# Kernel optimization log

Measured on AMD Instinct MI355X. Metric: run time of the kernel, lower is better.

The kernel has to match this reference:

```python
import jax, jax.numpy as jnp
import numpy as np

N_NODES = 100000
N_EDGES = 6400000


def _gcn_conv(x, src, dst, W, b, num_nodes):
    # GCNConv: x' = D^{-1/2} (A + I) D^{-1/2} X W + b
    # (src/dst already include self-loops; deg computed on A+I at dst, PyG default flow)
    h = x @ W  # [N, out]
    ones = jnp.ones(src.shape[0], dtype=h.dtype)
    deg = jax.ops.segment_sum(ones, dst, num_segments=num_nodes)  # in-degree incl. self-loops
    dinv = jnp.where(deg > 0, deg ** -0.5, 0.0)  # [N]
    norm = dinv[src] * dinv[dst]  # [E]
    msg = h[src] * norm[:, None]  # gather + scale, [E, out]
    agg = jax.ops.segment_sum(msg, dst, num_segments=num_nodes)  # scatter-add, [N, out]
    return agg + b


def setup_inputs() -> dict:
    key = jax.random.key(0)
    k1, k2, k3, k4 = jax.random.split(key, 4)
    x = jax.random.normal(k1, (N_NODES, 1), dtype=jnp.float32)
    edge_index = jax.random.randint(k2, (2, N_EDGES), 0, N_NODES, dtype=jnp.int64)
    # Glorot-style init for GCN weights
    W1 = jax.random.normal(k3, (1, 16), dtype=jnp.float32) * (2.0 / (1 + 16)) ** 0.5
    b1 = jnp.zeros((16,), dtype=jnp.float32)
    W2 = jax.random.normal(k4, (16, 2), dtype=jnp.float32) * (2.0 / (16 + 2)) ** 0.5
    b2 = jnp.zeros((2,), dtype=jnp.float32)
    return {"x": x, "edge_index": edge_index, "W1": W1, "b1": b1, "W2": W2, "b2": b2}


def reference(x, edge_index, W1, b1, W2, b2):
    num_nodes = x.shape[0]
    loops = jnp.arange(num_nodes, dtype=edge_index.dtype)
    src = jnp.concatenate([edge_index[0], loops])
    dst = jnp.concatenate([edge_index[1], loops])
    h = jax.nn.relu(_gcn_conv(x, src, dst, W1, b1, num_nodes))
    # F.dropout with training=False (eval) is identity
    out = _gcn_conv(h, src, dst, W2, b2, num_nodes)
    return jax.nn.log_softmax(out, axis=1)
```

## Files before the change

### kernel.cpp

```cpp
#include <hip/hip_runtime.h>
#include <hip/hip_fp16.h>

#define TPB 256
#define LOG_NPB 9
#define NPB 512
#define SPLIT 16
#define CHUNK 4096
#define RCAP 44


__device__ __forceinline__ void lds_pk_add_f16(unsigned* addr, unsigned val) {
  asm volatile("ds_pk_add_f16 %0, %1"
               :: "v"((unsigned)(unsigned long long)addr), "v"(val)
               : "memory");
}

__global__ void k_reset(int* __restrict__ gcur, int K) {
  int i = blockIdx.x * blockDim.x + threadIdx.x;
  if (i < K) gcur[i] = 0;
}

__global__ __launch_bounds__(TPB) void
k_bucket(const int* __restrict__ src, const int* __restrict__ dst,
         int E, int K, int capG,
         int* __restrict__ gcur, unsigned int* __restrict__ packed) {
  extern __shared__ unsigned smem[];
  unsigned* stage = smem;
  int* cur = (int*)(smem + (size_t)K * RCAP);
  int* res = cur + K;

  const int t = threadIdx.x;
  const int e0 = blockIdx.x * CHUNK;
  const int e1 = min(e0 + CHUNK, E);

  for (int b = t; b < K; b += TPB) cur[b] = 0;
  __syncthreads();

  for (int base = e0 + 4 * t; base < e1; base += 4 * TPB) {
    if (base + 4 <= e1) {
      int4 dv = *reinterpret_cast<const int4*>(dst + base);
      int4 sv = *reinterpret_cast<const int4*>(src + base);
      int d[4] = {dv.x, dv.y, dv.z, dv.w};
      int s[4] = {sv.x, sv.y, sv.z, sv.w};
#pragma unroll
      for (int j = 0; j < 4; ++j) {
        int b = d[j] >> LOG_NPB;
        unsigned pk = ((unsigned)s[j] << LOG_NPB) | (unsigned)(d[j] & (NPB - 1));
        int p = atomicAdd(&cur[b], 1);
        if (p < RCAP) {
          stage[b * RCAP + p] = pk;
        } else {
          int gp = atomicAdd(&gcur[b], 1);
          if (gp < capG) packed[(size_t)b * capG + gp] = pk;
        }
      }
    } else {
      for (int j = 0; j < 4; ++j) {
        int idx = base + j;
        if (idx < e1) {
          int d = dst[idx], s = src[idx];
          int b = d >> LOG_NPB;
          unsigned pk = ((unsigned)s << LOG_NPB) | (unsigned)(d & (NPB - 1));
          int p = atomicAdd(&cur[b], 1);
          if (p < RCAP) {
            stage[b * RCAP + p] = pk;
          } else {
            int gp = atomicAdd(&gcur[b], 1);
            if (gp < capG) packed[(size_t)b * capG + gp] = pk;
          }
        }
      }
    }
  }
  __syncthreads();

  if (t < K) {
    int c = min(cur[t], RCAP);
    res[t] = (c > 0) ? atomicAdd(&gcur[t], c) : 0;
  }
  __syncthreads();

  const int tot = K * RCAP;
  for (int i = t; i < tot; i += TPB) {
    int b = i / RCAP;
    int pos = i - b * RCAP;
    if (pos < min(cur[b], RCAP)) {
      int gp = res[b] + pos;
      if (gp < capG) packed[(size_t)b * capG + gp] = stage[i];
    }
  }
}

__device__ __forceinline__ void slice_range(int cnt, int s, int& off0, int& off1) {
  off0 = (int)(((long long)cnt * s) / SPLIT) & ~3;
  off1 = (s == SPLIT - 1) ? cnt : (int)(((long long)cnt * (s + 1)) / SPLIT) & ~3;
}

__global__ __launch_bounds__(TPB) void
k_deg(const unsigned int* __restrict__ packed, const int* __restrict__ gcur,
      int cap, int* __restrict__ pdeg, int Npad) {
  int b = blockIdx.x / SPLIT, s = blockIdx.x % SPLIT;
  __shared__ int bins[NPB];
  for (int i = threadIdx.x; i < NPB; i += TPB) bins[i] = 0;
  __syncthreads();
  int cnt = min(gcur[b], cap);
  int off0, off1; slice_range(cnt, s, off0, off1);
  const unsigned int* base = packed + (size_t)b * cap;
  int len = off1 - off0;
  int nfull = len >> 3;
  for (int g = threadIdx.x; g < nfull; g += TPB) {
    int e = off0 + (g << 3);
    uint4 pa = *reinterpret_cast<const uint4*>(base + e);
    uint4 pb = *reinterpret_cast<const uint4*>(base + e + 4);
    atomicAdd(&bins[pa.x & (NPB - 1)], 1);
    atomicAdd(&bins[pa.y & (NPB - 1)], 1);
    atomicAdd(&bins[pa.z & (NPB - 1)], 1);
    atomicAdd(&bins[pa.w & (NPB - 1)], 1);
    atomicAdd(&bins[pb.x & (NPB - 1)], 1);
    atomicAdd(&bins[pb.y & (NPB - 1)], 1);
    atomicAdd(&bins[pb.z & (NPB - 1)], 1);
    atomicAdd(&bins[pb.w & (NPB - 1)], 1);
  }
  for (int e = off0 + (nfull << 3) + threadIdx.x; e < off1; e += TPB)
    atomicAdd(&bins[base[e] & (NPB - 1)], 1);
  __syncthreads();
  int nb = b << LOG_NPB;
  for (int i = threadIdx.x; i < NPB; i += TPB)
    pdeg[s * Npad + nb + i] = bins[i];
}

__global__ void k_dinv(const int* __restrict__ pdeg, const float* __restrict__ x,
                       float* __restrict__ dinv, float* __restrict__ xd,
                       int N, int Npad) {
  int i = blockIdx.x * TPB + threadIdx.x;
  if (i >= N) return;
  int d = 1;
#pragma unroll
  for (int s = 0; s < SPLIT; ++s) d += pdeg[s * Npad + i];
  float di = rsqrtf((float)d);
  dinv[i] = di;
  xd[i] = x[i] * di;
}

__global__ __launch_bounds__(TPB) void
k_pass1(const unsigned int* __restrict__ packed, const int* __restrict__ gcur,
        int cap, const float* __restrict__ xd, float* __restrict__ pt1, int Npad) {
  int b = blockIdx.x / SPLIT, s = blockIdx.x % SPLIT;
  __shared__ float bins[NPB];
  for (int i = threadIdx.x; i < NPB; i += TPB) bins[i] = 0.f;
  __syncthreads();
  int cnt = min(gcur[b], cap);
  int off0, off1; slice_range(cnt, s, off0, off1);
  const unsigned int* base = packed + (size_t)b * cap;
  int len = off1 - off0;
  int nfull = len >> 3;
  for (int g = threadIdx.x; g < nfull; g += TPB) {
    int e = off0 + (g << 3);
    uint4 pa = *reinterpret_cast<const uint4*>(base + e);
    uint4 pb = *reinterpret_cast<const uint4*>(base + e + 4);
    float v0 = xd[pa.x >> LOG_NPB];
    float v1 = xd[pa.y >> LOG_NPB];
    float v2 = xd[pa.z >> LOG_NPB];
    float v3 = xd[pa.w >> LOG_NPB];
    float v4 = xd[pb.x >> LOG_NPB];
    float v5 = xd[pb.y >> LOG_NPB];
    float v6 = xd[pb.z >> LOG_NPB];
    float v7 = xd[pb.w >> LOG_NPB];
    atomicAdd(&bins[pa.x & (NPB - 1)], v0);
    atomicAdd(&bins[pa.y & (NPB - 1)], v1);
    atomicAdd(&bins[pa.z & (NPB - 1)], v2);
    atomicAdd(&bins[pa.w & (NPB - 1)], v3);
    atomicAdd(&bins[pb.x & (NPB - 1)], v4);
    atomicAdd(&bins[pb.y & (NPB - 1)], v5);
    atomicAdd(&bins[pb.z & (NPB - 1)], v6);
    atomicAdd(&bins[pb.w & (NPB - 1)], v7);
  }
  for (int e = off0 + (nfull << 3) + threadIdx.x; e < off1; e += TPB) {
    unsigned int p = base[e];
    atomicAdd(&bins[p & (NPB - 1)], xd[p >> LOG_NPB]);
  }
  __syncthreads();
  int nb = b << LOG_NPB;
  for (int i = threadIdx.x; i < NPB; i += TPB)
    pt1[s * Npad + nb + i] = bins[i];
}

__global__ void k_node(const float* __restrict__ pt1, const float* __restrict__ xd,
                       const float* __restrict__ dinv,
                       const float* __restrict__ W1, const float* __restrict__ b1,
                       const float* __restrict__ W2,
                       unsigned* __restrict__ gdp, int N, int Npad) {
  int i = blockIdx.x * TPB + threadIdx.x;
  if (i >= N) return;
  float tv = 0.f;
#pragma unroll
  for (int s = 0; s < SPLIT; ++s) tv += pt1[s * Npad + i];
  float di = dinv[i];
  float sv = di * (tv + xd[i]);
  float g0 = 0.f, g1 = 0.f;
#pragma unroll
  for (int j = 0; j < 16; ++j) {
    float h = fmaxf(fmaf(sv, W1[j], b1[j]), 0.f);
    g0 = fmaf(h, W2[2 * j], g0);
    g1 = fmaf(h, W2[2 * j + 1], g1);
  }
  __half2 h2 = __floats2half2_rn(g0 * di, g1 * di);
  gdp[i] = *reinterpret_cast<unsigned*>(&h2);
}

__global__ __launch_bounds__(TPB) void
k_pass2(const unsigned int* __restrict__ packed, const int* __restrict__ gcur,
        int cap, const unsigned* __restrict__ gdp, float* __restrict__ pt2, int Npad) {
  int b = blockIdx.x / SPLIT, s = blockIdx.x % SPLIT;
  __shared__ unsigned bins[NPB];
  for (int i = threadIdx.x; i < NPB; i += TPB) bins[i] = 0u;
  __syncthreads();
  int cnt = min(gcur[b], cap);
  int off0, off1; slice_range(cnt, s, off0, off1);
  const unsigned int* base = packed + (size_t)b * cap;
  int len = off1 - off0;
  int nfull = len >> 3;
  for (int g = threadIdx.x; g < nfull; g += TPB) {
    int e = off0 + (g << 3);
    uint4 pa = *reinterpret_cast<const uint4*>(base + e);
    uint4 pb = *reinterpret_cast<const uint4*>(base + e + 4);
    unsigned v0 = gdp[pa.x >> LOG_NPB];
    unsigned v1 = gdp[pa.y >> LOG_NPB];
    unsigned v2 = gdp[pa.z >> LOG_NPB];
    unsigned v3 = gdp[pa.w >> LOG_NPB];
    unsigned v4 = gdp[pb.x >> LOG_NPB];
    unsigned v5 = gdp[pb.y >> LOG_NPB];
    unsigned v6 = gdp[pb.z >> LOG_NPB];
    unsigned v7 = gdp[pb.w >> LOG_NPB];
    lds_pk_add_f16(&bins[pa.x & (NPB - 1)], v0);
    lds_pk_add_f16(&bins[pa.y & (NPB - 1)], v1);
    lds_pk_add_f16(&bins[pa.z & (NPB - 1)], v2);
    lds_pk_add_f16(&bins[pa.w & (NPB - 1)], v3);
    lds_pk_add_f16(&bins[pb.x & (NPB - 1)], v4);
    lds_pk_add_f16(&bins[pb.y & (NPB - 1)], v5);
    lds_pk_add_f16(&bins[pb.z & (NPB - 1)], v6);
    lds_pk_add_f16(&bins[pb.w & (NPB - 1)], v7);
  }
  for (int e = off0 + (nfull << 3) + threadIdx.x; e < off1; e += TPB) {
    unsigned int p = base[e];
    lds_pk_add_f16(&bins[p & (NPB - 1)], gdp[p >> LOG_NPB]);
  }
  __syncthreads();
  int nb = b << LOG_NPB;
  for (int i = threadIdx.x; i < NPB; i += TPB) {
    __half2 h = *reinterpret_cast<__half2*>(&bins[i]);
    float2 o;
    o.x = __low2float(h);
    o.y = __high2float(h);
    *reinterpret_cast<float2*>(pt2 + (size_t)s * 2 * Npad + 2 * (nb + i)) = o;
  }
}

__global__ void k_final(const float* __restrict__ pt2, const unsigned* __restrict__ gdp,
                        const float* __restrict__ dinv, const float* __restrict__ b2,
                        float* __restrict__ out, int N, int Npad) {
  int i = blockIdx.x * TPB + threadIdx.x;
  if (i >= N) return;
  float t0 = 0.f, t1 = 0.f;
#pragma unroll
  for (int s = 0; s < SPLIT; ++s) {
    float2 p = *reinterpret_cast<const float2*>(pt2 + (size_t)s * 2 * Npad + 2 * i);
    t0 += p.x;
    t1 += p.y;
  }
  unsigned gp = gdp[i];
  __half2 h = *reinterpret_cast<__half2*>(&gp);
  float di = dinv[i];
  float o0 = di * (t0 + __low2float(h)) + b2[0];
  float o1 = di * (t1 + __high2float(h)) + b2[1];
  float m = fmaxf(o0, o1);
  float l = m + logf(expf(o0 - m) + expf(o1 - m));
  out[2 * i] = o0 - l;
  out[2 * i + 1] = o1 - l;
}

extern "C" void kernel_launch(void* const* d_in, const int* in_sizes, int n_in,
                              void* d_out, int out_size, void* d_ws, size_t ws_size,
                              hipStream_t stream) {
  const float* x  = (const float*)d_in[0];
  const int*   ei = (const int*)d_in[1];
  const float* W1 = (const float*)d_in[2];
  const float* b1 = (const float*)d_in[3];
  const float* W2 = (const float*)d_in[4];
  const float* b2 = (const float*)d_in[5];

  const int N = in_sizes[0];
  const int E = in_sizes[1] / 2;
  const int* src = ei;
  const int* dst = ei + E;

  const int K = (N + NPB - 1) >> LOG_NPB;
  const int Npad = K << LOG_NPB;
  int mean = (int)(((long long)E * NPB) / N);
  int cap = mean + mean / 16 + 512;
  cap = (cap + 3) & ~3;

  char* ws = (char*)d_ws;
  auto align256 = [&](size_t n) { char* p = ws; ws += (n + 255) & ~(size_t)255; return p; };

  int*          gcur   = (int*)align256((size_t)K * 4);
  unsigned int* packed = (unsigned int*)align256((size_t)K * cap * 4);
  float*        dinv   = (float*)align256((size_t)N * 4);
  float*        xd     = (float*)align256((size_t)N * 4);
  unsigned*     gdp    = (unsigned*)align256((size_t)N * 4);
  float*        R      = (float*)align256((size_t)SPLIT * 2 * Npad * 4);
  int*          pdeg   = (int*)R;
  float*        pt1    = R;
  float*        pt2    = R;

  float* out = (float*)d_out;

  int nb_node   = (N + TPB - 1) / TPB;
  int nb_bucket = (E + CHUNK - 1) / CHUNK;
  int nb_acc    = K * SPLIT;
  size_t sh_bucket = ((size_t)K * RCAP + 2 * (size_t)K) * 4;

  k_reset <<<(K + TPB - 1) / TPB, TPB, 0, stream>>>(gcur, K);
  k_bucket<<<nb_bucket, TPB, sh_bucket, stream>>>(src, dst, E, K, cap, gcur, packed);
  k_deg   <<<nb_acc, TPB, 0, stream>>>(packed, gcur, cap, pdeg, Npad);
  k_dinv  <<<nb_node, TPB, 0, stream>>>(pdeg, x, dinv, xd, N, Npad);
  k_pass1 <<<nb_acc, TPB, 0, stream>>>(packed, gcur, cap, xd, pt1, Npad);
  k_node  <<<nb_node, TPB, 0, stream>>>(pt1, xd, dinv, W1, b1, W2, gdp, N, Npad);
  k_pass2 <<<nb_acc, TPB, 0, stream>>>(packed, gcur, cap, gdp, pt2, Npad);
  k_final <<<nb_node, TPB, 0, stream>>>(pt2, gdp, dinv, b2, out, N, Npad);
}
```

Baseline: 147.6 us.

## Pack degree and layer-1 partial sums into fp16 pairs with packed LDS atomics

The degree count and the first-layer scatter now accumulate into half2-packed LDS bins using ds_pk_add_f16, so two nodes share each bin word. Per-slice partials are written as packed fp16, which halves partial-buffer traffic in k_deg, k_dinv, k_pass1, k_node and k_final, and the node kernels each handle two nodes. The bucket kernel also loads 8 edges per thread and RCAP drops to 40. The risk is fp16 precision loss: per-slice degree counts are still exact, but the layer-1 partial sums of normalized features are rounded before the cross-slice sum.

New measurement: 174.3 us. 1.18x slower.

```diff
diff --git a/kernel.cpp b/kernel.cpp
--- a/kernel.cpp
+++ b/kernel.cpp
@@ -4,9 +4,10 @@
 #define TPB 256
 #define LOG_NPB 9
 #define NPB 512
+#define HPB 256
 #define SPLIT 16
 #define CHUNK 4096
-#define RCAP 44
+#define RCAP 40
 
 
 __device__ __forceinline__ void lds_pk_add_f16(unsigned* addr, unsigned val) {
@@ -36,14 +37,16 @@
   for (int b = t; b < K; b += TPB) cur[b] = 0;
   __syncthreads();
 
-  for (int base = e0 + 4 * t; base < e1; base += 4 * TPB) {
-    if (base + 4 <= e1) {
-      int4 dv = *reinterpret_cast<const int4*>(dst + base);
-      int4 sv = *reinterpret_cast<const int4*>(src + base);
-      int d[4] = {dv.x, dv.y, dv.z, dv.w};
-      int s[4] = {sv.x, sv.y, sv.z, sv.w};
-#pragma unroll
-      for (int j = 0; j < 4; ++j) {
+  for (int base = e0 + 8 * t; base < e1; base += 8 * TPB) {
+    if (base + 8 <= e1) {
+      int4 dv0 = *reinterpret_cast<const int4*>(dst + base);
+      int4 dv1 = *reinterpret_cast<const int4*>(dst + base + 4);
+      int4 sv0 = *reinterpret_cast<const int4*>(src + base);
+      int4 sv1 = *reinterpret_cast<const int4*>(src + base + 4);
+      int d[8] = {dv0.x, dv0.y, dv0.z, dv0.w, dv1.x, dv1.y, dv1.z, dv1.w};
+      int s[8] = {sv0.x, sv0.y, sv0.z, sv0.w, sv1.x, sv1.y, sv1.z, sv1.w};
+#pragma unroll
+      for (int j = 0; j < 8; ++j) {
         int b = d[j] >> LOG_NPB;
         unsigned pk = ((unsigned)s[j] << LOG_NPB) | (unsigned)(d[j] & (NPB - 1));
         int p = atomicAdd(&cur[b], 1);
@@ -55,19 +58,16 @@
         }
       }
     } else {
-      for (int j = 0; j < 4; ++j) {
-        int idx = base + j;
-        if (idx < e1) {
-          int d = dst[idx], s = src[idx];
-          int b = d >> LOG_NPB;
-          unsigned pk = ((unsigned)s << LOG_NPB) | (unsigned)(d & (NPB - 1));
-          int p = atomicAdd(&cur[b], 1);
-          if (p < RCAP) {
-            stage[b * RCAP + p] = pk;
-          } else {
-            int gp = atomicAdd(&gcur[b], 1);
-            if (gp < capG) packed[(size_t)b * capG + gp] = pk;
-          }
+      for (int idx = base; idx < e1; ++idx) {
+        int d = dst[idx], s = src[idx];
+        int b = d >> LOG_NPB;
+        unsigned pk = ((unsigned)s << LOG_NPB) | (unsigned)(d & (NPB - 1));
+        int p = atomicAdd(&cur[b], 1);
+        if (p < RCAP) {
+          stage[b * RCAP + p] = pk;
+        } else {
+          int gp = atomicAdd(&gcur[b], 1);
+          if (gp < capG) packed[(size_t)b * capG + gp] = pk;
         }
       }
     }
@@ -98,56 +98,65 @@
 
 __global__ __launch_bounds__(TPB) void
 k_deg(const unsigned int* __restrict__ packed, const int* __restrict__ gcur,
-      int cap, int* __restrict__ pdeg, int Npad) {
+      int cap, unsigned* __restrict__ pdeg_pk, int halfNpad) {
   int b = blockIdx.x / SPLIT, s = blockIdx.x % SPLIT;
-  __shared__ int bins[NPB];
-  for (int i = threadIdx.x; i < NPB; i += TPB) bins[i] = 0;
+  __shared__ unsigned binsp[HPB];
+  for (int i = threadIdx.x; i < HPB; i += TPB) binsp[i] = 0u;
   __syncthreads();
   int cnt = min(gcur[b], cap);
   int off0, off1; slice_range(cnt, s, off0, off1);
   const unsigned int* base = packed + (size_t)b * cap;
   int len = off1 - off0;
   int nfull = len >> 3;
+#define DEG1(P) { unsigned l_ = (P) & (NPB - 1); \
+  lds_pk_add_f16(&binsp[l_ >> 1], (l_ & 1) ? 0x3C000000u : 0x00003C00u); }
   for (int g = threadIdx.x; g < nfull; g += TPB) {
     int e = off0 + (g << 3);
     uint4 pa = *reinterpret_cast<const uint4*>(base + e);
     uint4 pb = *reinterpret_cast<const uint4*>(base + e + 4);
-    atomicAdd(&bins[pa.x & (NPB - 1)], 1);
-    atomicAdd(&bins[pa.y & (NPB - 1)], 1);
-    atomicAdd(&bins[pa.z & (NPB - 1)], 1);
-    atomicAdd(&bins[pa.w & (NPB - 1)], 1);
-    atomicAdd(&bins[pb.x & (NPB - 1)], 1);
-    atomicAdd(&bins[pb.y & (NPB - 1)], 1);
-    atomicAdd(&bins[pb.z & (NPB - 1)], 1);
-    atomicAdd(&bins[pb.w & (NPB - 1)], 1);
+    DEG1(pa.x) DEG1(pa.y) DEG1(pa.z) DEG1(pa.w)
+    DEG1(pb.x) DEG1(pb.y) DEG1(pb.z) DEG1(pb.w)
   }
   for (int e = off0 + (nfull << 3) + threadIdx.x; e < off1; e += TPB)
-    atomicAdd(&bins[base[e] & (NPB - 1)], 1);
-  __syncthreads();
-  int nb = b << LOG_NPB;
-  for (int i = threadIdx.x; i < NPB; i += TPB)
-    pdeg[s * Npad + nb + i] = bins[i];
-}
-
-__global__ void k_dinv(const int* __restrict__ pdeg, const float* __restrict__ x,
+    DEG1(base[e])
+#undef DEG1
+  __syncthreads();
+  int nb = b << (LOG_NPB - 1);
+  for (int i = threadIdx.x; i < HPB; i += TPB)
+    pdeg_pk[s * halfNpad + nb + i] = binsp[i];
+}
+
+__global__ void k_dinv(const unsigned* __restrict__ pdeg_pk, const float* __restrict__ x,
                        float* __restrict__ dinv, float* __restrict__ xd,
-                       int N, int Npad) {
-  int i = blockIdx.x * TPB + threadIdx.x;
-  if (i >= N) return;
-  int d = 1;
-#pragma unroll
-  for (int s = 0; s < SPLIT; ++s) d += pdeg[s * Npad + i];
-  float di = rsqrtf((float)d);
-  dinv[i] = di;
-  xd[i] = x[i] * di;
+                       int N, int halfNpad) {
+  int i2 = blockIdx.x * TPB + threadIdx.x;
+  int n0 = 2 * i2;
+  if (n0 >= N) return;
+  float d0 = 1.f, d1 = 1.f;
+#pragma unroll
+  for (int s = 0; s < SPLIT; ++s) {
+    unsigned v = pdeg_pk[s * halfNpad + i2];
+    __half2 h = *reinterpret_cast<__half2*>(&v);
+    d0 += __low2float(h);
+    d1 += __high2float(h);
+  }
+  float di0 = rsqrtf(d0);
+  dinv[n0] = di0;
+  xd[n0] = x[n0] * di0;
+  if (n0 + 1 < N) {
+    float di1 = rsqrtf(d1);
+    dinv[n0 + 1] = di1;
+    xd[n0 + 1] = x[n0 + 1] * di1;
+  }
 }
 
 __global__ __launch_bounds__(TPB) void
 k_pass1(const unsigned int* __restrict__ packed, const int* __restrict__ gcur,
-        int cap, const float* __restrict__ xd, float* __restrict__ pt1, int Npad) {
+        int cap, const float* __restrict__ xd, unsigned* __restrict__ pt1_pk,
+        int halfNpad) {
   int b = blockIdx.x / SPLIT, s = blockIdx.x % SPLIT;
-  __shared__ float bins[NPB];
-  for (int i = threadIdx.x; i < NPB; i += TPB) bins[i] = 0.f;
+  __shared__ unsigned binsp[HPB];
+  for (int i = threadIdx.x; i < HPB; i += TPB) binsp[i] = 0u;
   __syncthreads();
   int cnt = min(gcur[b], cap);
   int off0, off1; slice_range(cnt, s, off0, off1);
@@ -166,51 +175,71 @@
     float v5 = xd[pb.y >> LOG_NPB];
     float v6 = xd[pb.z >> LOG_NPB];
     float v7 = xd[pb.w >> LOG_NPB];
-    atomicAdd(&bins[pa.x & (NPB - 1)], v0);
-    atomicAdd(&bins[pa.y & (NPB - 1)], v1);
-    atomicAdd(&bins[pa.z & (NPB - 1)], v2);
-    atomicAdd(&bins[pa.w & (NPB - 1)], v3);
-    atomicAdd(&bins[pb.x & (NPB - 1)], v4);
-    atomicAdd(&bins[pb.y & (NPB - 1)], v5);
-    atomicAdd(&bins[pb.z & (NPB - 1)], v6);
-    atomicAdd(&bins[pb.w & (NPB - 1)], v7);
+#define P1(P, V) { unsigned l_ = (P) & (NPB - 1); \
+  unsigned hv_ = (unsigned)__half_as_ushort(__float2half(V)); \
+  lds_pk_add_f16(&binsp[l_ >> 1], hv_ << ((l_ & 1) * 16)); }
+    P1(pa.x, v0) P1(pa.y, v1) P1(pa.z, v2) P1(pa.w, v3)
+    P1(pb.x, v4) P1(pb.y, v5) P1(pb.z, v6) P1(pb.w, v7)
   }
   for (int e = off0 + (nfull << 3) + threadIdx.x; e < off1; e += TPB) {
-    unsigned int p = base[e];
-    atomicAdd(&bins[p & (NPB - 1)], xd[p >> LOG_NPB]);
-  }
-  __syncthreads();
-  int nb = b << LOG_NPB;
-  for (int i = threadIdx.x; i < NPB; i += TPB)
-    pt1[s * Npad + nb + i] = bins[i];
-}
-
-__global__ void k_node(const float* __restrict__ pt1, const float* __restrict__ xd,
+    unsigned p = base[e];
+    P1(p, xd[p >> LOG_NPB])
+  }
+#undef P1
+  __syncthreads();
+  int nb = b << (LOG_NPB - 1);
+  for (int i = threadIdx.x; i < HPB; i += TPB)
+    pt1_pk[s * halfNpad + nb + i] = binsp[i];
+}
+
+__global__ void k_node(const unsigned* __restrict__ pt1_pk, const float* __restrict__ xd,
                        const float* __restrict__ dinv,
                        const float* __restrict__ W1, const float* __restrict__ b1,
                        const float* __restrict__ W2,
-                       unsigned* __restrict__ gdp, int N, int Npad) {
-  int i = blockIdx.x * TPB + threadIdx.x;
-  if (i >= N) return;
-  float tv = 0.f;
-#pragma unroll
-  for (int s = 0; s < SPLIT; ++s) tv += pt1[s * Npad + i];
-  float di = dinv[i];
-  float sv = di * (tv + xd[i]);
-  float g0 = 0.f, g1 = 0.f;
-#pragma unroll
-  for (int j = 0; j < 16; ++j) {
-    float h = fmaxf(fmaf(sv, W1[j], b1[j]), 0.f);
-    g0 = fmaf(h, W2[2 * j], g0);
-    g1 = fmaf(h, W2[2 * j + 1], g1);
-  }
-  __half2 h2 = __floats2half2_rn(g0 * di, g1 * di);
-  gdp[i] = *reinterpret_cast<unsigned*>(&h2);
+                       unsigned* __restrict__ gdp, int N, int halfNpad) {
+  int i2 = blockIdx.x * TPB + threadIdx.x;
+  int n0 = 2 * i2;
+  if (n0 >= N) return;
+  float t0 = 0.f, t1 = 0.f;
+#pragma unroll
+  for (int s = 0; s < SPLIT; ++s) {
+    unsigned v = pt1_pk[s * halfNpad + i2];
+    __half2 h = *reinterpret_cast<__half2*>(&v);
+    t0 += __low2float(h);
+    t1 += __high2float(h);
+  }
+  {
+    float di = dinv[n0];
+    float sv = di * (t0 + xd[n0]);
+    float g0 = 0.f, g1 = 0.f;
+#pragma unroll
+    for (int j = 0; j < 16; ++j) {
+      float h = fmaxf(fmaf(sv, W1[j], b1[j]), 0.f);
+      g0 = fmaf(h, W2[2 * j], g0);
+      g1 = fmaf(h, W2[2 * j + 1], g1);
+    }
+    __half2 h2 = __floats2half2_rn(g0 * di, g1 * di);
+    gdp[n0] = *reinterpret_cast<unsigned*>(&h2);
+  }
+  if (n0 + 1 < N) {
+    float di = dinv[n0 + 1];
+    float sv = di * (t1 + xd[n0 + 1]);
+    float g0 = 0.f, g1 = 0.f;
+#pragma unroll
+    for (int j = 0; j < 16; ++j) {
+      float h = fmaxf(fmaf(sv, W1[j], b1[j]), 0.f);
+      g0 = fmaf(h, W2[2 * j], g0);
+      g1 = fmaf(h, W2[2 * j + 1], g1);
+    }
+    __half2 h2 = __floats2half2_rn(g0 * di, g1 * di);
+    gdp[n0 + 1] = *reinterpret_cast<unsigned*>(&h2);
+  }
 }
 
 __global__ __launch_bounds__(TPB) void
 k_pass2(const unsigned int* __restrict__ packed, const int* __restrict__ gcur,
-        int cap, const unsigned* __restrict__ gdp, float* __restrict__ pt2, int Npad) {
+        int cap, const unsigned* __restrict__ gdp, unsigned* __restrict__ pt2_pk,
+        int Npad) {
   int b = blockIdx.x / SPLIT, s = blockIdx.x % SPLIT;
   __shared__ unsigned bins[NPB];
   for (int i = threadIdx.x; i < NPB; i += TPB) bins[i] = 0u;
@@ -247,16 +276,11 @@
   }
   __syncthreads();
   int nb = b << LOG_NPB;
-  for (int i = threadIdx.x; i < NPB; i += TPB) {
-    __half2 h = *reinterpret_cast<__half2*>(&bins[i]);
-    float2 o;
-    o.x = __low2float(h);
-    o.y = __high2float(h);
-    *reinterpret_cast<float2*>(pt2 + (size_t)s * 2 * Npad + 2 * (nb + i)) = o;
-  }
-}
-
-__global__ void k_final(const float* __restrict__ pt2, const unsigned* __restrict__ gdp,
+  for (int i = threadIdx.x; i < NPB; i += TPB)
+    pt2_pk[(size_t)s * Npad + nb + i] = bins[i];
+}
+
+__global__ void k_final(const unsigned* __restrict__ pt2_pk, const unsigned* __restrict__ gdp,
                         const float* __restrict__ dinv, const float* __restrict__ b2,
                         float* __restrict__ out, int N, int Npad) {
   int i = blockIdx.x * TPB + threadIdx.x;
@@ -264,9 +288,10 @@
   float t0 = 0.f, t1 = 0.f;
 #pragma unroll
   for (int s = 0; s < SPLIT; ++s) {
-    float2 p = *reinterpret_cast<const float2*>(pt2 + (size_t)s * 2 * Npad + 2 * i);
-    t0 += p.x;
-    t1 += p.y;
+    unsigned v = pt2_pk[(size_t)s * Npad + i];
+    __half2 h = *reinterpret_cast<__half2*>(&v);
+    t0 += __low2float(h);
+    t1 += __high2float(h);
   }
   unsigned gp = gdp[i];
   __half2 h = *reinterpret_cast<__half2*>(&gp);
@@ -296,6 +321,7 @@
 
   const int K = (N + NPB - 1) >> LOG_NPB;
   const int Npad = K << LOG_NPB;
+  const int halfNpad = Npad >> 1;
   int mean = (int)(((long long)E * NPB) / N);
   int cap = mean + mean / 16 + 512;
   cap = (cap + 3) & ~3;
@@ -308,13 +334,14 @@
   float*        dinv   = (float*)align256((size_t)N * 4);
   float*        xd     = (float*)align256((size_t)N * 4);
   unsigned*     gdp    = (unsigned*)align256((size_t)N * 4);
-  float*        R      = (float*)align256((size_t)SPLIT * 2 * Npad * 4);
-  int*          pdeg   = (int*)R;
-  float*        pt1    = R;
-  float*        pt2    = R;
+  unsigned*     R      = (unsigned*)align256((size_t)SPLIT * Npad * 4);
+  unsigned*     pdeg_pk = R;
+  unsigned*     pt1_pk  = R;
+  unsigned*     pt2_pk  = R;
 
   float* out = (float*)d_out;
 
+  int nb_pair   = ((N + 1) / 2 + TPB - 1) / TPB;
   int nb_node   = (N + TPB - 1) / TPB;
   int nb_bucket = (E + CHUNK - 1) / CHUNK;
   int nb_acc    = K * SPLIT;
@@ -322,10 +349,10 @@
 
   k_reset <<<(K + TPB - 1) / TPB, TPB, 0, stream>>>(gcur, K);
   k_bucket<<<nb_bucket, TPB, sh_bucket, stream>>>(src, dst, E, K, cap, gcur, packed);
-  k_deg   <<<nb_acc, TPB, 0, stream>>>(packed, gcur, cap, pdeg, Npad);
-  k_dinv  <<<nb_node, TPB, 0, stream>>>(pdeg, x, dinv, xd, N, Npad);
-  k_pass1 <<<nb_acc, TPB, 0, stream>>>(packed, gcur, cap, xd, pt1, Npad);
-  k_node  <<<nb_node, TPB, 0, stream>>>(pt1, xd, dinv, W1, b1, W2, gdp, N, Npad);
-  k_pass2 <<<nb_acc, TPB, 0, stream>>>(packed, gcur, cap, gdp, pt2, Npad);
-  k_final <<<nb_node, TPB, 0, stream>>>(pt2, gdp, dinv, b2, out, N, Npad);
-}
+  k_deg   <<<nb_acc, TPB, 0, stream>>>(packed, gcur, cap, pdeg_pk, halfNpad);
+  k_dinv  <<<nb_pair, TPB, 0, stream>>>(pdeg_pk, x, dinv, xd, N, halfNpad);
+  k_pass1 <<<nb_acc, TPB, 0, stream>>>(packed, gcur, cap, xd, pt1_pk, halfNpad);
+  k_node  <<<nb_pair, TPB, 0, stream>>>(pt1_pk, xd, dinv, W1, b1, W2, gdp, N, halfNpad);
+  k_pass2 <<<nb_acc, TPB, 0, stream>>>(packed, gcur, cap, gdp, pt2_pk, Npad);
+  k_final <<<nb_node, TPB, 0, stream>>>(pt2_pk, gdp, dinv, b2, out, N, Npad);
+}
```
